# Optimization experiments

Measured on AMD Instinct MI355X. Metric: run time of the kernel, lower is better.

Reference implementation:

```python
import jax, jax.numpy as jnp
import numpy as np

E = 128          # emb_dim
H = 128          # hidden_size (== emb_dim, forced by theta7)
B = 2048         # batch_size (number of graphs)
MAXN = 64        # max_possible_nodes; every graph uses all 64 nodes
N = B * MAXN     # total nodes = 131072


def setup_inputs() -> dict:
    key = jax.random.key(0)
    ks = jax.random.split(key, 16)
    s = 0.05
    return {
        "mu_raw": jax.random.normal(ks[0], (1, N, E), jnp.float32),
        "h0": jax.random.normal(ks[1], (1, N, H), jnp.float32) * s,
        "c0": jax.random.normal(ks[2], (1, N, H), jnp.float32) * s,
        "batch_ids": jnp.repeat(jnp.arange(B, dtype=jnp.int32), MAXN),
        "reachable": jax.random.randint(ks[3], (N,), 0, 2).astype(bool),
        "W_ih": jax.random.normal(ks[4], (4 * H, E), jnp.float32) * s,
        "W_hh": jax.random.normal(ks[5], (4 * H, H), jnp.float32) * s,
        "b_ih": jnp.zeros((4 * H,), jnp.float32),
        "b_hh": jnp.zeros((4 * H,), jnp.float32),
        "W5": jax.random.normal(ks[6], (1, 2 * E), jnp.float32) * s,
        "b5": jnp.zeros((1,), jnp.float32),
        "W6": jax.random.normal(ks[7], (E, E), jnp.float32) * s,
        "b6": jnp.zeros((E,), jnp.float32),
        "W7": jax.random.normal(ks[8], (E, E), jnp.float32) * s,
        "b7": jnp.zeros((E,), jnp.float32),
    }


def reference(mu_raw, h0, c0, batch_ids, reachable,
              W_ih, W_hh, b_ih, b_hh, W5, b5, W6, b6, W7, b7):
    x = mu_raw[0]               # [N, E]  (seq_len == 1)
    hp, cp = h0[0], c0[0]       # [N, H]
    # Single LSTM step; torch gate order: input, forget, cell(g), output
    gates = x @ W_ih.T + b_ih + hp @ W_hh.T + b_hh      # [N, 4H]
    i, f, g, o = jnp.split(gates, 4, axis=-1)
    i, f, o = jax.nn.sigmoid(i), jax.nn.sigmoid(f), jax.nn.sigmoid(o)
    g = jnp.tanh(g)
    c = f * cp + i * g
    h = o * jnp.tanh(c)                                  # mu_mem [N, H]
    # scatter_mean over graph ids
    sums = jax.ops.segment_sum(h, batch_ids, num_segments=B)            # [B, H]
    cnt = jax.ops.segment_sum(jnp.ones((N, 1), h.dtype), batch_ids, num_segments=B)
    mean = sums / jnp.maximum(cnt, 1.0)
    # repeat_interleave by nodes-per-graph == gather by batch id
    gexp = mean[batch_ids]                               # [N, H]
    global_state = gexp @ W6.T + b6
    local_action = h @ W7.T + b7
    rep = jax.nn.relu(jnp.concatenate([global_state, local_action], axis=-1))  # [N, 2E]
    logits = (rep @ W5.T + b5)[:, 0]                     # [N]
    logits = jnp.where(reachable, logits, -jnp.inf)
    # uniform graphs: split/pad -> simple reshape to [1, B, MAXN]
    return logits.reshape(1, B, MAXN)
```

## Files before the change

kernel.cpp:

```cpp
#include <hip/hip_runtime.h>
#include <math.h>

#define MASK_NEG 3.0e38f

typedef _Float16 f16x8 __attribute__((ext_vector_type(8)));
typedef float    f32x4 __attribute__((ext_vector_type(4)));

#define SWZ(byte, row) ((byte) ^ (((row) & 7) << 4))

__device__ __forceinline__ f16x8 cvt8(float4 a, float4 b) {
    f16x8 h;
    h[0]=(_Float16)a.x; h[1]=(_Float16)a.y; h[2]=(_Float16)a.z; h[3]=(_Float16)a.w;
    h[4]=(_Float16)b.x; h[5]=(_Float16)b.y; h[6]=(_Float16)b.z; h[7]=(_Float16)b.w;
    return h;
}

__launch_bounds__(512, 2)
__global__ void fused_kernel(const float* __restrict__ x, const float* __restrict__ h0,
                             const float* __restrict__ c0, const unsigned char* __restrict__ reach,
                             const float* __restrict__ Wih, const float* __restrict__ Whh,
                             const float* __restrict__ bih, const float* __restrict__ bhh,
                             const float* __restrict__ W5, const float* __restrict__ b5v,
                             const float* __restrict__ W6, const float* __restrict__ b6,
                             const float* __restrict__ W7, const float* __restrict__ b7,
                             float* __restrict__ out) {
    __shared__ __align__(16) _Float16 As[128 * 256];
    __shared__ __align__(16) _Float16 Hs[128 * 128];
    __shared__ float mean_s[2][128];
    __shared__ float sG_s[2];

    const int t    = threadIdx.x;
    const int lane = t & 63;
    const int w    = t >> 6;
    const int l15  = lane & 15;
    const int l4   = lane >> 4;
    const int row0 = blockIdx.x * 128;
    const int j    = w * 16 + l15;

    if (t < 2) sG_s[t] = b5v[0];

    #pragma unroll
    for (int c = 0; c < 4; ++c) {
        int flat = c * 4096 + t * 8;
        int r    = flat >> 7;
        int col  = flat & 127;
        size_t g = (size_t)(row0 + r) * 128 + col;
        float4 a0 = *(const float4*)(x + g);
        float4 a1 = *(const float4*)(x + g + 4);
        float4 b0 = *(const float4*)(h0 + g);
        float4 b1 = *(const float4*)(h0 + g + 4);
        int byteA = r * 512 + col * 2;
        int byteB = r * 512 + (128 + col) * 2;
        *(f16x8*)((char*)As + SWZ(byteA, r)) = cvt8(a0, a1);
        *(f16x8*)((char*)As + SWZ(byteB, r)) = cvt8(b0, b1);
    }

    const float* cpbase = c0 + (size_t)row0 * 128 + j;
    float cpn0, cpn1, cpn2, cpn3;
    {
        const float* cp = cpbase + (size_t)(l4 * 4) * 128;
        cpn0 = cp[0]; cpn1 = cp[128]; cpn2 = cp[256]; cpn3 = cp[384];
    }

    f16x8 bfr[4][8];
    {
        #pragma unroll
        for (int gt = 0; gt < 4; ++gt) {
            const float* ri = Wih + (size_t)(gt * 128 + j) * 128 + l4 * 8;
            const float* rh = Whh + (size_t)(gt * 128 + j) * 128 + l4 * 8;
            #pragma unroll
            for (int kf = 0; kf < 4; ++kf) {
                float4 a = *(const float4*)(ri + kf * 32);
                float4 b = *(const float4*)(ri + kf * 32 + 4);
                bfr[gt][kf] = cvt8(a, b);
            }
            #pragma unroll
            for (int kf = 0; kf < 4; ++kf) {
                float4 a = *(const float4*)(rh + kf * 32);
                float4 b = *(const float4*)(rh + kf * 32 + 4);
                bfr[gt][kf + 4] = cvt8(a, b);
            }
        }
    }
    float bg[4];
    #pragma unroll
    for (int gt = 0; gt < 4; ++gt) bg[gt] = bih[gt * 128 + j] + bhh[gt * 128 + j];

    __syncthreads();

    float gsum0 = 0.f, gsum1 = 0.f;
    #pragma unroll 1
    for (int s = 0; s < 8; ++s) {
        float cpr0 = cpn0, cpr1 = cpn1, cpr2 = cpn2, cpr3 = cpn3;
        if (s < 7) {
            const float* cp = cpbase + (size_t)((s + 1) * 16 + l4 * 4) * 128;
            cpn0 = cp[0]; cpn1 = cp[128]; cpn2 = cp[256]; cpn3 = cp[384];
        }

        f16x8 af[8];
        int rr = s * 16 + l15;
        #pragma unroll
        for (int kf = 0; kf < 8; ++kf) {
            int byte = rr * 512 + kf * 64 + l4 * 16;
            af[kf] = *(const f16x8*)((char*)As + SWZ(byte, rr));
        }

        f32x4 acc0 = {0,0,0,0}, acc1 = {0,0,0,0}, acc2 = {0,0,0,0}, acc3 = {0,0,0,0};
        #pragma unroll
        for (int kf = 0; kf < 8; ++kf) {
            acc0 = __builtin_amdgcn_mfma_f32_16x16x32_f16(af[kf], bfr[0][kf], acc0, 0, 0, 0);
            acc1 = __builtin_amdgcn_mfma_f32_16x16x32_f16(af[kf], bfr[1][kf], acc1, 0, 0, 0);
            acc2 = __builtin_amdgcn_mfma_f32_16x16x32_f16(af[kf], bfr[2][kf], acc2, 0, 0, 0);
            acc3 = __builtin_amdgcn_mfma_f32_16x16x32_f16(af[kf], bfr[3][kf], acc3, 0, 0, 0);
        }
        int mbase = s * 16 + l4 * 4;
        float hsum = 0.f;
        #pragma unroll
        for (int r = 0; r < 4; ++r) {
            float cprv = (r == 0) ? cpr0 : (r == 1) ? cpr1 : (r == 2) ? cpr2 : cpr3;
            float gi = acc0[r] + bg[0];
            float gf = acc1[r] + bg[1];
            float gg = acc2[r] + bg[2];
            float go = acc3[r] + bg[3];
            float iv = 1.f / (1.f + __expf(-gi));
            float fv = 1.f / (1.f + __expf(-gf));
            float gv = 1.f - 2.f / (__expf(2.f * gg) + 1.f);
            float ov = 1.f / (1.f + __expf(-go));
            float cc = fv * cprv + iv * gv;
            float th = 1.f - 2.f / (__expf(2.f * cc) + 1.f);
            float hh = ov * th;
            hsum += hh;
            int hrow  = mbase + r;
            int hbyte = hrow * 256 + j * 2;
            *(_Float16*)((char*)Hs + SWZ(hbyte, hrow)) = (_Float16)hh;
        }
        hsum += __shfl_xor(hsum, 16, 64);
        hsum += __shfl_xor(hsum, 32, 64);
        if (s < 4) gsum0 += hsum; else gsum1 += hsum;
    }

    if (lane < 16) {
        mean_s[0][w * 16 + lane] = gsum0 * (1.f / 64.f);
        mean_s[1][w * 16 + lane] = gsum1 * (1.f / 64.f);
    }
    __syncthreads();

    if (t < 256) {
        int g = t >> 7, jj = t & 127;
        const float* w6r = W6 + jj * 128;
        float a = 0.f;
        #pragma unroll 8
        for (int k = 0; k < 128; k += 4) {
            float4 wv = *(const float4*)(w6r + k);
            a += mean_s[g][k] * wv.x + mean_s[g][k + 1] * wv.y
               + mean_s[g][k + 2] * wv.z + mean_s[g][k + 3] * wv.w;
        }
        a += b6[jj];
        float contrib = fmaxf(a, 0.f) * W5[jj];
        #pragma unroll
        for (int m = 1; m < 64; m <<= 1) contrib += __shfl_xor(contrib, m, 64);
        if (lane == 0) atomicAdd(&sG_s[g], contrib);
    }

    f16x8 af2[4];
    {
        int rr = j;
        #pragma unroll
        for (int kf = 0; kf < 4; ++kf) {
            int byte = rr * 256 + kf * 64 + l4 * 16;
            af2[kf] = *(const f16x8*)((char*)Hs + SWZ(byte, rr));
        }
    }
    f32x4 lacc[8];
    #pragma unroll
    for (int nt = 0; nt < 8; ++nt) {
        f32x4 a = {0, 0, 0, 0};
        const float* w7r = W7 + (size_t)(nt * 16 + l15) * 128 + l4 * 8;
        #pragma unroll
        for (int kf = 0; kf < 4; ++kf) {
            float4 p = *(const float4*)(w7r + kf * 32);
            float4 q = *(const float4*)(w7r + kf * 32 + 4);
            a = __builtin_amdgcn_mfma_f32_16x16x32_f16(af2[kf], cvt8(p, q), a, 0, 0, 0);
        }
        lacc[nt] = a;
    }

    __syncthreads();

    float sGv = sG_s[w >> 2];
    float rs0 = 0.f, rs1 = 0.f, rs2 = 0.f, rs3 = 0.f;
    #pragma unroll
    for (int nt = 0; nt < 8; ++nt) {
        int n = nt * 16 + l15;
        float b7n = b7[n];
        float w5n = W5[128 + n];
        rs0 += fmaxf(lacc[nt][0] + b7n, 0.f) * w5n;
        rs1 += fmaxf(lacc[nt][1] + b7n, 0.f) * w5n;
        rs2 += fmaxf(lacc[nt][2] + b7n, 0.f) * w5n;
        rs3 += fmaxf(lacc[nt][3] + b7n, 0.f) * w5n;
    }
    #pragma unroll
    for (int m = 1; m < 16; m <<= 1) {
        rs0 += __shfl_xor(rs0, m, 64);
        rs1 += __shfl_xor(rs1, m, 64);
        rs2 += __shfl_xor(rs2, m, 64);
        rs3 += __shfl_xor(rs3, m, 64);
    }
    if (l15 == 0) {
        int mg = row0 + w * 16 + l4 * 4;
        float v0 = sGv + rs0, v1 = sGv + rs1, v2 = sGv + rs2, v3 = sGv + rs3;
        out[mg + 0] = reach[mg + 0] ? v0 : -MASK_NEG;
        out[mg + 1] = reach[mg + 1] ? v1 : -MASK_NEG;
        out[mg + 2] = reach[mg + 2] ? v2 : -MASK_NEG;
        out[mg + 3] = reach[mg + 3] ? v3 : -MASK_NEG;
    }
}

extern "C" void kernel_launch(void* const* d_in, const int* in_sizes, int n_in,
                              void* d_out, int out_size, void* d_ws, size_t ws_size,
                              hipStream_t stream) {
    const float* mu  = (const float*)d_in[0];
    const float* h0  = (const float*)d_in[1];
    const float* c0  = (const float*)d_in[2];
    const unsigned char* reach = (const unsigned char*)d_in[4];
    const float* Wih = (const float*)d_in[5];
    const float* Whh = (const float*)d_in[6];
    const float* bih = (const float*)d_in[7];
    const float* bhh = (const float*)d_in[8];
    const float* W5  = (const float*)d_in[9];
    const float* b5  = (const float*)d_in[10];
    const float* W6  = (const float*)d_in[11];
    const float* b6  = (const float*)d_in[12];
    const float* W7  = (const float*)d_in[13];
    const float* b7  = (const float*)d_in[14];
    float* out = (float*)d_out;

    int N      = in_sizes[0] / 128;
    int blocks = N / 128;

    hipLaunchKernelGGL(fused_kernel, dim3(blocks), dim3(512), 0, stream,
                       mu, h0, c0, reach, Wih, Whh, bih, bhh, W5, b5, W6, b6, W7, b7, out);
}
```

Before: 372.6 us.

## Make fused LSTM kernel persistent with register prefetch of next tile and LDS-resident W7

Launches a fixed grid of 256 blocks that loop over 128-row tiles. Each block loads and converts the gate weights once, stages W7 in LDS as fp16, and prefetches the next tile's x/h0 into registers while the current tile finishes its epilogue. The goal is to amortise the per-block weight loads and hide global-load latency behind compute. In exchange it uses more registers and LDS, which may cut occupancy, and the grid is capped at 256 blocks, which may not fill every CU.

```diff
diff --git a/kernel.cpp b/kernel.cpp
--- a/kernel.cpp
+++ b/kernel.cpp
@@ -13,6 +13,12 @@
     h[0]=(_Float16)a.x; h[1]=(_Float16)a.y; h[2]=(_Float16)a.z; h[3]=(_Float16)a.w;
     h[4]=(_Float16)b.x; h[5]=(_Float16)b.y; h[6]=(_Float16)b.z; h[7]=(_Float16)b.w;
     return h;
+}
+
+__device__ __forceinline__ void bar_lgkm() {
+    asm volatile("s_waitcnt lgkmcnt(0)" ::: "memory");
+    __builtin_amdgcn_s_barrier();
+    __builtin_amdgcn_sched_barrier(0);
 }
 
 __launch_bounds__(512, 2)
@@ -23,197 +29,234 @@
                              const float* __restrict__ W5, const float* __restrict__ b5v,
                              const float* __restrict__ W6, const float* __restrict__ b6,
                              const float* __restrict__ W7, const float* __restrict__ b7,
-                             float* __restrict__ out) {
+                             float* __restrict__ out, int ntiles) {
     __shared__ __align__(16) _Float16 As[128 * 256];
     __shared__ __align__(16) _Float16 Hs[128 * 128];
+    __shared__ __align__(16) _Float16 W7s[128 * 128];
     __shared__ float mean_s[2][128];
-    __shared__ float sG_s[2];
+    __shared__ float sG_s[4];
 
     const int t    = threadIdx.x;
     const int lane = t & 63;
     const int w    = t >> 6;
     const int l15  = lane & 15;
     const int l4   = lane >> 4;
-    const int row0 = blockIdx.x * 128;
-    const int j    = w * 16 + l15;
-
-    if (t < 2) sG_s[t] = b5v[0];
-
+    const int jcol = w * 16 + l15;
+
+    float4 xr[8], hr[8];
+    f16x8  xh[8];
+
+#define PREFETCH(tt) do {                                                   \
+        size_t gbase = (size_t)(tt) * 16384;                                \
+        _Pragma("unroll")                                                   \
+        for (int c = 0; c < 4; ++c) {                                       \
+            size_t g = gbase + c * 4096 + t * 8;                            \
+            xr[2*c]   = *(const float4*)(x + g);                            \
+            xr[2*c+1] = *(const float4*)(x + g + 4);                        \
+            hr[2*c]   = *(const float4*)(h0 + g);                           \
+            hr[2*c+1] = *(const float4*)(h0 + g + 4);                       \
+        }                                                                   \
+    } while (0)
+
+#define CONVERT() do {                                                      \
+        _Pragma("unroll")                                                   \
+        for (int c = 0; c < 4; ++c) {                                       \
+            xh[c]     = cvt8(xr[2*c], xr[2*c+1]);                           \
+            xh[4 + c] = cvt8(hr[2*c], hr[2*c+1]);                           \
+        }                                                                   \
+    } while (0)
+
+    PREFETCH(blockIdx.x);
+
+    f16x8 bfr[4][8];
     #pragma unroll
-    for (int c = 0; c < 4; ++c) {
-        int flat = c * 4096 + t * 8;
-        int r    = flat >> 7;
-        int col  = flat & 127;
-        size_t g = (size_t)(row0 + r) * 128 + col;
-        float4 a0 = *(const float4*)(x + g);
-        float4 a1 = *(const float4*)(x + g + 4);
-        float4 b0 = *(const float4*)(h0 + g);
-        float4 b1 = *(const float4*)(h0 + g + 4);
-        int byteA = r * 512 + col * 2;
-        int byteB = r * 512 + (128 + col) * 2;
-        *(f16x8*)((char*)As + SWZ(byteA, r)) = cvt8(a0, a1);
-        *(f16x8*)((char*)As + SWZ(byteB, r)) = cvt8(b0, b1);
-    }
-
-    const float* cpbase = c0 + (size_t)row0 * 128 + j;
-    float cpn0, cpn1, cpn2, cpn3;
-    {
-        const float* cp = cpbase + (size_t)(l4 * 4) * 128;
-        cpn0 = cp[0]; cpn1 = cp[128]; cpn2 = cp[256]; cpn3 = cp[384];
-    }
-
-    f16x8 bfr[4][8];
-    {
-        #pragma unroll
-        for (int gt = 0; gt < 4; ++gt) {
-            const float* ri = Wih + (size_t)(gt * 128 + j) * 128 + l4 * 8;
-            const float* rh = Whh + (size_t)(gt * 128 + j) * 128 + l4 * 8;
-            #pragma unroll
-            for (int kf = 0; kf < 4; ++kf) {
-                float4 a = *(const float4*)(ri + kf * 32);
-                float4 b = *(const float4*)(ri + kf * 32 + 4);
-                bfr[gt][kf] = cvt8(a, b);
-            }
-            #pragma unroll
-            for (int kf = 0; kf < 4; ++kf) {
-                float4 a = *(const float4*)(rh + kf * 32);
-                float4 b = *(const float4*)(rh + kf * 32 + 4);
-                bfr[gt][kf + 4] = cvt8(a, b);
-            }
-        }
+    for (int gt = 0; gt < 4; ++gt) {
+        const float* ri = Wih + (size_t)(gt * 128 + jcol) * 128 + l4 * 8;
+        const float* rh = Whh + (size_t)(gt * 128 + jcol) * 128 + l4 * 8;
+        #pragma unroll
+        for (int kf = 0; kf < 4; ++kf)
+            bfr[gt][kf] = cvt8(*(const float4*)(ri + kf * 32),
+                               *(const float4*)(ri + kf * 32 + 4));
+        #pragma unroll
+        for (int kf = 0; kf < 4; ++kf)
+            bfr[gt][kf + 4] = cvt8(*(const float4*)(rh + kf * 32),
+                                   *(const float4*)(rh + kf * 32 + 4));
     }
     float bg[4];
     #pragma unroll
-    for (int gt = 0; gt < 4; ++gt) bg[gt] = bih[gt * 128 + j] + bhh[gt * 128 + j];
-
-    __syncthreads();
-
-    float gsum0 = 0.f, gsum1 = 0.f;
-    #pragma unroll 1
-    for (int s = 0; s < 8; ++s) {
-        float cpr0 = cpn0, cpr1 = cpn1, cpr2 = cpn2, cpr3 = cpn3;
-        if (s < 7) {
-            const float* cp = cpbase + (size_t)((s + 1) * 16 + l4 * 4) * 128;
+    for (int gt = 0; gt < 4; ++gt) bg[gt] = bih[gt * 128 + jcol] + bhh[gt * 128 + jcol];
+
+    {
+        int r = t >> 2, cb = (t & 3) * 32;
+        #pragma unroll
+        for (int q = 0; q < 2; ++q) {
+            int col = cb + q * 16;
+            const float* src = W7 + (size_t)r * 128 + col;
+            f16x8 v0 = cvt8(*(const float4*)(src),     *(const float4*)(src + 4));
+            f16x8 v1 = cvt8(*(const float4*)(src + 8), *(const float4*)(src + 12));
+            int byte0 = r * 256 + col * 2;
+            *(f16x8*)((char*)W7s + SWZ(byte0, r))      = v0;
+            *(f16x8*)((char*)W7s + SWZ(byte0 + 16, r)) = v1;
+        }
+    }
+
+    CONVERT();
+
+    int pp = 0;
+    for (int tile = blockIdx.x; tile < ntiles; tile += gridDim.x, pp ^= 1) {
+        const int row0 = tile * 128;
+        float* sg = &sG_s[pp * 2];
+        if (t < 2) sg[t] = b5v[0];
+
+        #pragma unroll
+        for (int c = 0; c < 4; ++c) {
+            int flat = c * 4096 + t * 8;
+            int r    = flat >> 7;
+            int col  = flat & 127;
+            int byteA = r * 512 + col * 2;
+            int byteB = r * 512 + (128 + col) * 2;
+            *(f16x8*)((char*)As + SWZ(byteA, r)) = xh[c];
+            *(f16x8*)((char*)As + SWZ(byteB, r)) = xh[4 + c];
+        }
+
+        const float* cpbase = c0 + (size_t)row0 * 128 + jcol;
+        float cpn0, cpn1, cpn2, cpn3;
+        {
+            const float* cp = cpbase + (size_t)(l4 * 4) * 128;
             cpn0 = cp[0]; cpn1 = cp[128]; cpn2 = cp[256]; cpn3 = cp[384];
         }
-
-        f16x8 af[8];
-        int rr = s * 16 + l15;
-        #pragma unroll
-        for (int kf = 0; kf < 8; ++kf) {
-            int byte = rr * 512 + kf * 64 + l4 * 16;
-            af[kf] = *(const f16x8*)((char*)As + SWZ(byte, rr));
-        }
-
-        f32x4 acc0 = {0,0,0,0}, acc1 = {0,0,0,0}, acc2 = {0,0,0,0}, acc3 = {0,0,0,0};
-        #pragma unroll
-        for (int kf = 0; kf < 8; ++kf) {
-            acc0 = __builtin_amdgcn_mfma_f32_16x16x32_f16(af[kf], bfr[0][kf], acc0, 0, 0, 0);
-            acc1 = __builtin_amdgcn_mfma_f32_16x16x32_f16(af[kf], bfr[1][kf], acc1, 0, 0, 0);
-            acc2 = __builtin_amdgcn_mfma_f32_16x16x32_f16(af[kf], bfr[2][kf], acc2, 0, 0, 0);
-            acc3 = __builtin_amdgcn_mfma_f32_16x16x32_f16(af[kf], bfr[3][kf], acc3, 0, 0, 0);
-        }
-        int mbase = s * 16 + l4 * 4;
-        float hsum = 0.f;
-        #pragma unroll
-        for (int r = 0; r < 4; ++r) {
-            float cprv = (r == 0) ? cpr0 : (r == 1) ? cpr1 : (r == 2) ? cpr2 : cpr3;
-            float gi = acc0[r] + bg[0];
-            float gf = acc1[r] + bg[1];
-            float gg = acc2[r] + bg[2];
-            float go = acc3[r] + bg[3];
-            float iv = 1.f / (1.f + __expf(-gi));
-            float fv = 1.f / (1.f + __expf(-gf));
-            float gv = 1.f - 2.f / (__expf(2.f * gg) + 1.f);
-            float ov = 1.f / (1.f + __expf(-go));
-            float cc = fv * cprv + iv * gv;
-            float th = 1.f - 2.f / (__expf(2.f * cc) + 1.f);
-            float hh = ov * th;
-            hsum += hh;
-            int hrow  = mbase + r;
-            int hbyte = hrow * 256 + j * 2;
-            *(_Float16*)((char*)Hs + SWZ(hbyte, hrow)) = (_Float16)hh;
-        }
-        hsum += __shfl_xor(hsum, 16, 64);
-        hsum += __shfl_xor(hsum, 32, 64);
-        if (s < 4) gsum0 += hsum; else gsum1 += hsum;
+        bar_lgkm();
+
+        float gsum0 = 0.f, gsum1 = 0.f;
+        #pragma unroll 1
+        for (int s = 0; s < 8; ++s) {
+            float cpr0 = cpn0, cpr1 = cpn1, cpr2 = cpn2, cpr3 = cpn3;
+            if (s < 7) {
+                const float* cp = cpbase + (size_t)((s + 1) * 16 + l4 * 4) * 128;
+                cpn0 = cp[0]; cpn1 = cp[128]; cpn2 = cp[256]; cpn3 = cp[384];
+            }
+
+            f16x8 af[8];
+            int rr = s * 16 + l15;
+            #pragma unroll
+            for (int kf = 0; kf < 8; ++kf) {
+                int byte = rr * 512 + kf * 64 + l4 * 16;
+                af[kf] = *(const f16x8*)((char*)As + SWZ(byte, rr));
+            }
+
+            f32x4 acc0 = {0,0,0,0}, acc1 = {0,0,0,0}, acc2 = {0,0,0,0}, acc3 = {0,0,0,0};
+            #pragma unroll
+            for (int kf = 0; kf < 8; ++kf) {
+                acc0 = __builtin_amdgcn_mfma_f32_16x16x32_f16(af[kf], bfr[0][kf], acc0, 0, 0, 0);
+                acc1 = __builtin_amdgcn_mfma_f32_16x16x32_f16(af[kf], bfr[1][kf], acc1, 0, 0, 0);
+                acc2 = __builtin_amdgcn_mfma_f32_16x16x32_f16(af[kf], bfr[2][kf], acc2, 0, 0, 0);
+                acc3 = __builtin_amdgcn_mfma_f32_16x16x32_f16(af[kf], bfr[3][kf], acc3, 0, 0, 0);
+            }
+            int mbase = s * 16 + l4 * 4;
+            float hsum = 0.f;
+            #pragma unroll
+            for (int r = 0; r < 4; ++r) {
+                float cprv = (r == 0) ? cpr0 : (r == 1) ? cpr1 : (r == 2) ? cpr2 : cpr3;
+                float gi = acc0[r] + bg[0];
+                float gf = acc1[r] + bg[1];
+                float gg = acc2[r] + bg[2];
+                float go = acc3[r] + bg[3];
+                float iv = 1.f / (1.f + __expf(-gi));
+                float fv = 1.f / (1.f + __expf(-gf));
+                float gv = 1.f - 2.f / (__expf(2.f * gg) + 1.f);
+                float ov = 1.f / (1.f + __expf(-go));
+                float cc = fv * cprv + iv * gv;
+                float th = 1.f - 2.f / (__expf(2.f * cc) + 1.f);
+                float hh = ov * th;
+                hsum += hh;
+                int hrow  = mbase + r;
+                int hbyte = hrow * 256 + jcol * 2;
+                *(_Float16*)((char*)Hs + SWZ(hbyte, hrow)) = (_Float16)hh;
+            }
+            hsum += __shfl_xor(hsum, 16, 64);
+            hsum += __shfl_xor(hsum, 32, 64);
+            if (s < 4) gsum0 += hsum; else gsum1 += hsum;
+        }
+
+        const bool hasNext = (tile + (int)gridDim.x) < ntiles;
+        if (hasNext) PREFETCH(tile + gridDim.x);
+
+        if (lane < 16) {
+            mean_s[0][w * 16 + lane] = gsum0 * (1.f / 64.f);
+            mean_s[1][w * 16 + lane] = gsum1 * (1.f / 64.f);
+        }
+        bar_lgkm();
+
+        if (t < 256) {
+            int g = t >> 7, jj = t & 127;
+            const float* w6r = W6 + jj * 128;
+            float a = 0.f;
+            #pragma unroll 8
+            for (int k = 0; k < 128; k += 4) {
+                float4 wv = *(const float4*)(w6r + k);
+                a += mean_s[g][k] * wv.x + mean_s[g][k + 1] * wv.y
+                   + mean_s[g][k + 2] * wv.z + mean_s[g][k + 3] * wv.w;
+            }
+            a += b6[jj];
+            float contrib = fmaxf(a, 0.f) * W5[jj];
+            #pragma unroll
+            for (int m = 1; m < 64; m <<= 1) contrib += __shfl_xor(contrib, m, 64);
+            if (lane == 0) atomicAdd(&sg[g], contrib);
+        }
+
+        if (hasNext) CONVERT();
+
+        f16x8 af2[4];
+        #pragma unroll
+        for (int kf = 0; kf < 4; ++kf) {
+            int byte = jcol * 256 + kf * 64 + l4 * 16;
+            af2[kf] = *(const f16x8*)((char*)Hs + SWZ(byte, jcol));
+        }
+        f32x4 lacc[8];
+        #pragma unroll
+        for (int nt = 0; nt < 8; ++nt) {
+            f32x4 a = {0, 0, 0, 0};
+            int n = nt * 16 + l15;
+            #pragma unroll
+            for (int kf = 0; kf < 4; ++kf) {
+                int byte = n * 256 + kf * 64 + l4 * 16;
+                f16x8 bf = *(const f16x8*)((char*)W7s + SWZ(byte, n));
+                a = __builtin_amdgcn_mfma_f32_16x16x32_f16(af2[kf], bf, a, 0, 0, 0);
+            }
+            lacc[nt] = a;
+        }
+        bar_lgkm();
+
+        float sGv = sg[w >> 2];
+        float rs0 = 0.f, rs1 = 0.f, rs2 = 0.f, rs3 = 0.f;
+        #pragma unroll
+        for (int nt = 0; nt < 8; ++nt) {
+            int n = nt * 16 + l15;
+            float b7n = b7[n];
+            float w5n = W5[128 + n];
+            rs0 += fmaxf(lacc[nt][0] + b7n, 0.f) * w5n;
+            rs1 += fmaxf(lacc[nt][1] + b7n, 0.f) * w5n;
+            rs2 += fmaxf(lacc[nt][2] + b7n, 0.f) * w5n;
+            rs3 += fmaxf(lacc[nt][3] + b7n, 0.f) * w5n;
+        }
+        #pragma unroll
+        for (int m = 1; m < 16; m <<= 1) {
+            rs0 += __shfl_xor(rs0, m, 64);
+            rs1 += __shfl_xor(rs1, m, 64);
+            rs2 += __shfl_xor(rs2, m, 64);
+            rs3 += __shfl_xor(rs3, m, 64);
+        }
+        if (l15 == 0) {
+            int mg = row0 + w * 16 + l4 * 4;
+            float v0 = sGv + rs0, v1 = sGv + rs1, v2 = sGv + rs2, v3 = sGv + rs3;
+            out[mg + 0] = reach[mg + 0] ? v0 : -MASK_NEG;
+            out[mg + 1] = reach[mg + 1] ? v1 : -MASK_NEG;
+            out[mg + 2] = reach[mg + 2] ? v2 : -MASK_NEG;
+            out[mg + 3] = reach[mg + 3] ? v3 : -MASK_NEG;
+        }
     }
-
-    if (lane < 16) {
-        mean_s[0][w * 16 + lane] = gsum0 * (1.f / 64.f);
-        mean_s[1][w * 16 + lane] = gsum1 * (1.f / 64.f);
-    }
-    __syncthreads();
-
-    if (t < 256) {
-        int g = t >> 7, jj = t & 127;
-        const float* w6r = W6 + jj * 128;
-        float a = 0.f;
-        #pragma unroll 8
-        for (int k = 0; k < 128; k += 4) {
-            float4 wv = *(const float4*)(w6r + k);
-            a += mean_s[g][k] * wv.x + mean_s[g][k + 1] * wv.y
-               + mean_s[g][k + 2] * wv.z + mean_s[g][k + 3] * wv.w;
-        }
-        a += b6[jj];
-        float contrib = fmaxf(a, 0.f) * W5[jj];
-        #pragma unroll
-        for (int m = 1; m < 64; m <<= 1) contrib += __shfl_xor(contrib, m, 64);
-        if (lane == 0) atomicAdd(&sG_s[g], contrib);
-    }
-
-    f16x8 af2[4];
-    {
-        int rr = j;
-        #pragma unroll
-        for (int kf = 0; kf < 4; ++kf) {
-            int byte = rr * 256 + kf * 64 + l4 * 16;
-            af2[kf] = *(const f16x8*)((char*)Hs + SWZ(byte, rr));
-        }
-    }
-    f32x4 lacc[8];
-    #pragma unroll
-    for (int nt = 0; nt < 8; ++nt) {
-        f32x4 a = {0, 0, 0, 0};
-        const float* w7r = W7 + (size_t)(nt * 16 + l15) * 128 + l4 * 8;
-        #pragma unroll
-        for (int kf = 0; kf < 4; ++kf) {
-            float4 p = *(const float4*)(w7r + kf * 32);
-            float4 q = *(const float4*)(w7r + kf * 32 + 4);
-            a = __builtin_amdgcn_mfma_f32_16x16x32_f16(af2[kf], cvt8(p, q), a, 0, 0, 0);
-        }
-        lacc[nt] = a;
-    }
-
-    __syncthreads();
-
-    float sGv = sG_s[w >> 2];
-    float rs0 = 0.f, rs1 = 0.f, rs2 = 0.f, rs3 = 0.f;
-    #pragma unroll
-    for (int nt = 0; nt < 8; ++nt) {
-        int n = nt * 16 + l15;
-        float b7n = b7[n];
-        float w5n = W5[128 + n];
-        rs0 += fmaxf(lacc[nt][0] + b7n, 0.f) * w5n;
-        rs1 += fmaxf(lacc[nt][1] + b7n, 0.f) * w5n;
-        rs2 += fmaxf(lacc[nt][2] + b7n, 0.f) * w5n;
-        rs3 += fmaxf(lacc[nt][3] + b7n, 0.f) * w5n;
-    }
-    #pragma unroll
-    for (int m = 1; m < 16; m <<= 1) {
-        rs0 += __shfl_xor(rs0, m, 64);
-        rs1 += __shfl_xor(rs1, m, 64);
-        rs2 += __shfl_xor(rs2, m, 64);
-        rs3 += __shfl_xor(rs3, m, 64);
-    }
-    if (l15 == 0) {
-        int mg = row0 + w * 16 + l4 * 4;
-        float v0 = sGv + rs0, v1 = sGv + rs1, v2 = sGv + rs2, v3 = sGv + rs3;
-        out[mg + 0] = reach[mg + 0] ? v0 : -MASK_NEG;
-        out[mg + 1] = reach[mg + 1] ? v1 : -MASK_NEG;
-        out[mg + 2] = reach[mg + 2] ? v2 : -MASK_NEG;
-        out[mg + 3] = reach[mg + 3] ? v3 : -MASK_NEG;
-    }
+#undef PREFETCH
+#undef CONVERT
 }
 
 extern "C" void kernel_launch(void* const* d_in, const int* in_sizes, int n_in,
@@ -236,8 +279,10 @@
     float* out = (float*)d_out;
 
     int N      = in_sizes[0] / 128;
-    int blocks = N / 128;
+    int ntiles = N / 128;
+    int blocks = ntiles < 256 ? ntiles : 256;
 
     hipLaunchKernelGGL(fused_kernel, dim3(blocks), dim3(512), 0, stream,
-                       mu, h0, c0, reach, Wih, Whh, bih, bhh, W5, b5, W6, b6, W7, b7, out);
-}
+                       mu, h0, c0, reach, Wih, Whh, bih, bhh, W5, b5, W6, b6, W7, b7,
+                       out, ntiles);
+}
```

Measured after the change: 353.9 us. -5.0%, faster.
